# Performance work log

Hardware: AMD Instinct MI355X
Metric: run time of the kernel (lower is better)

## Reference

```python
import jax, jax.numpy as jnp
import numpy as np

MAX_ITER = 16
TOL = 1e-3


def setup_inputs() -> dict:
    key = jax.random.key(0)
    k0, k1, k2, k3 = jax.random.split(key, 4)
    B, A, Bd, Y = 16384, 1024, 2, 128
    AT = jax.random.uniform(k0, (B, A), dtype=jnp.float32)
    K = jax.random.uniform(k1, (A, Bd), dtype=jnp.float32)
    BT = jnp.ones((Bd,), dtype=jnp.float32)  # fixed to [1, 1] in the module
    u = jax.random.uniform(k2, (A * Bd, Y), dtype=jnp.float32)
    b = jax.random.uniform(k3, (Y,), dtype=jnp.float32)
    return {"AT": AT, "K": K, "BT": BT, "u": u, "b": b}


def reference(AT, K, BT, u, b):
    batch = AT.shape[0]
    Kp = K ** 2  # 'reparam' constraint

    # Fixed-point matrix-balancing loop (torch.no_grad block) -> constants.
    Ksg = jax.lax.stop_gradient(Kp)
    ATsg = jax.lax.stop_gradient(AT)
    A_dim, B_dim = Kp.shape
    af0 = jnp.zeros((batch, A_dim), jnp.float32)
    bf0 = jnp.zeros((batch, B_dim), jnp.float32)

    def cond(carry):
        _, _, err, i = carry
        return (i < MAX_ITER) & (err >= TOL)

    def body(carry):
        af, bf, _, i = carry
        af_n = ATsg / (bf @ Ksg.T + 1.0)   # (batch, A_dim)
        bf_n = BT / (af_n @ Ksg + 1.0)     # (batch, B_dim)
        err = jnp.max(jnp.abs(af_n - af)) + jnp.max(jnp.abs(bf_n - bf))
        return af_n, bf_n, err, i + 1

    _, bf, _, _ = jax.lax.while_loop(
        cond, body, (af0, bf0, jnp.array(jnp.inf, jnp.float32), 0)
    )
    bf = jax.lax.stop_gradient(bf)

    # Final differentiable iteration.
    af = AT / (bf @ Kp.T + 1.0)            # (batch, A_dim)
    bf = BT / (af @ Kp + 1.0)              # (batch, B_dim)

    # C = K * (AF @ BF^T): rank-1 outer product per batch element.
    C = (Kp[None, :, :] * af[:, :, None] * bf[:, None, :]).reshape(batch, -1)
    return C @ u + b
```

## Files before the change

### kernel.cpp

```cpp
#include <hip/hip_runtime.h>

__device__ __forceinline__ float b2f(unsigned short h) {
    unsigned int u = ((unsigned int)h) << 16;
    return __builtin_bit_cast(float, u);
}
__device__ __forceinline__ unsigned short f2b(float f) {
    unsigned int u = __builtin_bit_cast(unsigned int, f);
    u += 0x7fffu + ((u >> 16) & 1u);
    return (unsigned short)(u >> 16);
}

typedef short bf16x8_t __attribute__((ext_vector_type(8)));
typedef float f32x4_t  __attribute__((ext_vector_type(4)));

#define LDS_PTR(p) ((__attribute__((address_space(3))) void*)(p))
#define GLB_PTR(p) ((const __attribute__((address_space(1))) void*)(p))

#define NB   16384
#define AD   1024
#define YD   128
#define ND   256

__global__ __launch_bounds__(256) void vt_kernel(
    const float* __restrict__ Kq,
    const float* __restrict__ U,
    unsigned short* __restrict__ Vt)
{
    int idx = blockIdx.x * 256 + threadIdx.x;
    int n = idx >> 10;
    int a = idx & 1023;
    int j = n >> 7;
    int y = n & 127;
    float k  = Kq[2 * a + j];
    float kp = k * k;
    float uv = U[(size_t)(2 * a + j) * YD + y];
    Vt[idx] = f2b(kp * uv);
}

__global__ __launch_bounds__(256) void row_kernel(
    const float* __restrict__ AT,
    const float* __restrict__ Kq,
    const float* __restrict__ BTv,
    unsigned short* __restrict__ afb,
    float* __restrict__ bff)
{
    int wid  = blockIdx.x * 4 + (threadIdx.x >> 6);
    int lane = threadIdx.x & 63;
    const float* at = AT + (size_t)wid * AD;

    float ta[16], kp0[16], kp1[16];
#pragma unroll
    for (int c = 0; c < 4; ++c) {
        int base = c * 256 + lane * 4;
        float4 av = *(const float4*)(at + base);
        ta[c * 4 + 0] = av.x; ta[c * 4 + 1] = av.y;
        ta[c * 4 + 2] = av.z; ta[c * 4 + 3] = av.w;
        float4 k0 = *(const float4*)(Kq + 2 * base);
        float4 k1 = *(const float4*)(Kq + 2 * base + 4);
        kp0[c * 4 + 0] = k0.x * k0.x; kp1[c * 4 + 0] = k0.y * k0.y;
        kp0[c * 4 + 1] = k0.z * k0.z; kp1[c * 4 + 1] = k0.w * k0.w;
        kp0[c * 4 + 2] = k1.x * k1.x; kp1[c * 4 + 2] = k1.y * k1.y;
        kp0[c * 4 + 3] = k1.z * k1.z; kp1[c * 4 + 3] = k1.w * k1.w;
    }

    float M[9];
#pragma unroll
    for (int i = 0; i < 9; ++i) M[i] = 0.f;
#pragma unroll
    for (int e = 0; e < 16; ++e) {
        float t = ta[e], p = kp0[e], q = kp1[e];
        float u0 = t * p, u1 = t * q;
        M[0] += u0; M[1] += u1;
        float u00 = u0 * p, u01 = u0 * q, u11 = u1 * q;
        M[2] += u00; M[3] += u01; M[4] += u11;
        M[5] += u00 * p; M[6] += u00 * q; M[7] += u01 * q; M[8] += u11 * q;
    }
#pragma unroll
    for (int i = 0; i < 9; ++i) {
        for (int m = 1; m < 64; m <<= 1) M[i] += __shfl_xor(M[i], m, 64);
    }

    float bt0 = BTv[0], bt1 = BTv[1];
    float bf0 = 0.f, bf1 = 0.f;
#pragma unroll
    for (int it = 0; it < 8; ++it) {
        float q00 = bf0 * bf0, q01 = bf0 * bf1, q11 = bf1 * bf1;
        float s0 = M[0] - (bf0 * M[2] + bf1 * M[3]) + (q00 * M[5] + 2.f * q01 * M[6] + q11 * M[7]);
        float s1 = M[1] - (bf0 * M[3] + bf1 * M[4]) + (q00 * M[6] + 2.f * q01 * M[7] + q11 * M[8]);
        bf0 = bt0 / (1.f + s0);
        bf1 = bt1 / (1.f + s1);
    }
    if (lane == 0) { bff[(size_t)wid * 2] = bf0; bff[(size_t)wid * 2 + 1] = bf1; }

    unsigned short* ao = afb + (size_t)wid * AD;
#pragma unroll
    for (int c = 0; c < 4; ++c) {
        unsigned short r[4];
#pragma unroll
        for (int e = 0; e < 4; ++e) {
            int idx = c * 4 + e;
            r[e] = f2b(ta[idx] / (1.f + bf0 * kp0[idx] + bf1 * kp1[idx]));
        }
        *(ushort4*)(ao + c * 256 + lane * 4) = make_ushort4(r[0], r[1], r[2], r[3]);
    }
}

__global__ __launch_bounds__(256) void gemm_kernel(
    const unsigned short* __restrict__ Ag,
    const unsigned short* __restrict__ Bg,
    float* __restrict__ G)
{
    __shared__ __align__(16) unsigned short lA[128 * 64];
    __shared__ __align__(16) unsigned short lB[128 * 64];

    const int t = threadIdx.x;
    const int lane = t & 63;
    const int wave = t >> 6;
    const int wm = wave >> 1, wn = wave & 1;
    const int mtile = blockIdx.x, ntile = blockIdx.y;

    f32x4_t acc[4][4];
#pragma unroll
    for (int i = 0; i < 4; ++i)
#pragma unroll
        for (int j = 0; j < 4; ++j) acc[i][j] = (f32x4_t){0.f, 0.f, 0.f, 0.f};

    const unsigned short* gA[4];
    const unsigned short* gB[4];
    int ls[4];
#pragma unroll
    for (int i = 0; i < 4; ++i) {
        int s = i * 256 + t;
        int m = s >> 3;
        int c = (s & 7) ^ (m & 7);
        gA[i] = Ag + (size_t)(mtile * 128 + m) * AD + 8 * c;
        gB[i] = Bg + (size_t)(ntile * 128 + m) * AD + 8 * c;
        ls[i] = s * 8;
    }

    for (int k0 = 0; k0 < AD; k0 += 64) {
#pragma unroll
        for (int i = 0; i < 4; ++i) {
            __builtin_amdgcn_global_load_lds(GLB_PTR(gA[i] + k0), LDS_PTR(&lA[ls[i]]), 16, 0, 0);
            __builtin_amdgcn_global_load_lds(GLB_PTR(gB[i] + k0), LDS_PTR(&lB[ls[i]]), 16, 0, 0);
        }
        __syncthreads();
#pragma unroll
        for (int kk = 0; kk < 2; ++kk) {
            const int cq = kk * 4 + (lane >> 4);
            const int rr = lane & 15;
            bf16x8_t fa[4], fb[4];
#pragma unroll
            for (int i = 0; i < 4; ++i) {
                int m = wm * 64 + i * 16 + rr;
                fa[i] = *(const bf16x8_t*)(&lA[(m * 8 + (cq ^ (m & 7))) * 8]);
                int n = wn * 64 + i * 16 + rr;
                fb[i] = *(const bf16x8_t*)(&lB[(n * 8 + (cq ^ (n & 7))) * 8]);
            }
#pragma unroll
            for (int i = 0; i < 4; ++i)
#pragma unroll
                for (int j = 0; j < 4; ++j)
                    acc[i][j] = __builtin_amdgcn_mfma_f32_16x16x32_bf16(fa[i], fb[j], acc[i][j], 0, 0, 0);
        }
        __syncthreads();
    }

    const int q = lane >> 4, col = lane & 15;
#pragma unroll
    for (int i = 0; i < 4; ++i) {
        int mg = mtile * 128 + wm * 64 + i * 16 + q * 4;
#pragma unroll
        for (int j = 0; j < 4; ++j) {
            int ng = ntile * 128 + wn * 64 + j * 16 + col;
            float* gp = G + (size_t)mg * ND + ng;
#pragma unroll
            for (int r = 0; r < 4; ++r) gp[(size_t)r * ND] = acc[i][j][r];
        }
    }
}

__global__ __launch_bounds__(256) void combine_kernel(
    const float* __restrict__ G,
    const float* __restrict__ bff,
    const float* __restrict__ bias,
    float* __restrict__ out)
{
    int idx = blockIdx.x * 256 + threadIdx.x;
    int b  = idx >> 5;
    int y4 = (idx & 31) * 4;
    float bf0 = bff[2 * b], bf1 = bff[2 * b + 1];
    float4 g0 = *(const float4*)(G + (size_t)b * ND + y4);
    float4 g1 = *(const float4*)(G + (size_t)b * ND + YD + y4);
    float4 bv = *(const float4*)(bias + y4);
    float4 r;
    r.x = bf0 * g0.x + bf1 * g1.x + bv.x;
    r.y = bf0 * g0.y + bf1 * g1.y + bv.y;
    r.z = bf0 * g0.z + bf1 * g1.z + bv.z;
    r.w = bf0 * g0.w + bf1 * g1.w + bv.w;
    *(float4*)(out + (size_t)b * YD + y4) = r;
}

extern "C" void kernel_launch(void* const* d_in, const int* in_sizes, int n_in,
                              void* d_out, int out_size, void* d_ws, size_t ws_size,
                              hipStream_t stream) {
    const float* AT  = (const float*)d_in[0];
    const float* Kq  = (const float*)d_in[1];
    const float* BTv = (const float*)d_in[2];
    const float* U   = (const float*)d_in[3];
    const float* bia = (const float*)d_in[4];
    float* out = (float*)d_out;

    char* ws = (char*)d_ws;
    unsigned short* afb = (unsigned short*)(ws);
    unsigned short* Vt  = (unsigned short*)(ws + 33554432);
    float*          G   = (float*)(ws + 34078720);
    float*          bff = (float*)(ws + 50855936);

    vt_kernel<<<dim3(1024), dim3(256), 0, stream>>>(Kq, U, Vt);
    row_kernel<<<dim3(NB / 4), dim3(256), 0, stream>>>(AT, Kq, BTv, afb, bff);
    gemm_kernel<<<dim3(NB / 128, ND / 128), dim3(256), 0, stream>>>(afb, Vt, G);
    combine_kernel<<<dim3(NB * 32 / 256), dim3(256), 0, stream>>>(G, bff, bia, out);
}
```

Before: 140.6 us.

## Fuse combine epilogue into GEMM with full-N tiles per block

The GEMM now uses 32-row M tiles that span all 256 N columns, so each block holds both halves (j=0 and j=1) for the same output column. This lets it apply the bf weighting and bias in the epilogue and write the final output directly. The separate combine kernel and the 16 MB G intermediate round trip are removed. In exchange, every block reloads the full 256x1024 B matrix (likely served from L2), and each wave issues fewer MFMAs per LDS load, which lowers arithmetic intensity.

New measurement: 129.8 us. 7.7% less time.

```diff
diff --git a/kernel.cpp b/kernel.cpp
--- a/kernel.cpp
+++ b/kernel.cpp
@@ -105,60 +105,66 @@
     }
 }
 
-__global__ __launch_bounds__(256) void gemm_kernel(
+__global__ __launch_bounds__(256) void gemm_fused_kernel(
     const unsigned short* __restrict__ Ag,
     const unsigned short* __restrict__ Bg,
-    float* __restrict__ G)
+    const float* __restrict__ bff,
+    const float* __restrict__ bias,
+    float* __restrict__ out)
 {
-    __shared__ __align__(16) unsigned short lA[128 * 64];
-    __shared__ __align__(16) unsigned short lB[128 * 64];
+    __shared__ __align__(16) unsigned short lA[32 * 64];
+    __shared__ __align__(16) unsigned short lB[256 * 64];
 
     const int t = threadIdx.x;
     const int lane = t & 63;
-    const int wave = t >> 6;
-    const int wm = wave >> 1, wn = wave & 1;
-    const int mtile = blockIdx.x, ntile = blockIdx.y;
-
-    f32x4_t acc[4][4];
-#pragma unroll
-    for (int i = 0; i < 4; ++i)
+    const int wn = t >> 6;
+    const int mtile = blockIdx.x;
+
+    f32x4_t acc[2][4];
+#pragma unroll
+    for (int i = 0; i < 2; ++i)
 #pragma unroll
         for (int j = 0; j < 4; ++j) acc[i][j] = (f32x4_t){0.f, 0.f, 0.f, 0.f};
 
-    const unsigned short* gA[4];
-    const unsigned short* gB[4];
-    int ls[4];
-#pragma unroll
-    for (int i = 0; i < 4; ++i) {
-        int s = i * 256 + t;
+    const unsigned short* gA;
+    const unsigned short* gB[8];
+    {
+        int s = t;
         int m = s >> 3;
         int c = (s & 7) ^ (m & 7);
-        gA[i] = Ag + (size_t)(mtile * 128 + m) * AD + 8 * c;
-        gB[i] = Bg + (size_t)(ntile * 128 + m) * AD + 8 * c;
-        ls[i] = s * 8;
+        gA = Ag + (size_t)(mtile * 32 + m) * AD + 8 * c;
+    }
+#pragma unroll
+    for (int i = 0; i < 8; ++i) {
+        int s = i * 256 + t;
+        int n = s >> 3;
+        int c = (s & 7) ^ (n & 7);
+        gB[i] = Bg + (size_t)n * AD + 8 * c;
     }
 
     for (int k0 = 0; k0 < AD; k0 += 64) {
-#pragma unroll
-        for (int i = 0; i < 4; ++i) {
-            __builtin_amdgcn_global_load_lds(GLB_PTR(gA[i] + k0), LDS_PTR(&lA[ls[i]]), 16, 0, 0);
-            __builtin_amdgcn_global_load_lds(GLB_PTR(gB[i] + k0), LDS_PTR(&lB[ls[i]]), 16, 0, 0);
-        }
+        __builtin_amdgcn_global_load_lds(GLB_PTR(gA + k0), LDS_PTR(&lA[t * 8]), 16, 0, 0);
+#pragma unroll
+        for (int i = 0; i < 8; ++i)
+            __builtin_amdgcn_global_load_lds(GLB_PTR(gB[i] + k0), LDS_PTR(&lB[(i * 256 + t) * 8]), 16, 0, 0);
         __syncthreads();
 #pragma unroll
         for (int kk = 0; kk < 2; ++kk) {
             const int cq = kk * 4 + (lane >> 4);
             const int rr = lane & 15;
-            bf16x8_t fa[4], fb[4];
-#pragma unroll
-            for (int i = 0; i < 4; ++i) {
-                int m = wm * 64 + i * 16 + rr;
+            bf16x8_t fa[2], fb[4];
+#pragma unroll
+            for (int i = 0; i < 2; ++i) {
+                int m = i * 16 + rr;
                 fa[i] = *(const bf16x8_t*)(&lA[(m * 8 + (cq ^ (m & 7))) * 8]);
-                int n = wn * 64 + i * 16 + rr;
-                fb[i] = *(const bf16x8_t*)(&lB[(n * 8 + (cq ^ (n & 7))) * 8]);
             }
 #pragma unroll
-            for (int i = 0; i < 4; ++i)
+            for (int j = 0; j < 4; ++j) {
+                int n = wn * 32 + (j & 1) * 16 + (j >> 1) * 128 + rr;
+                fb[j] = *(const bf16x8_t*)(&lB[(n * 8 + (cq ^ (n & 7))) * 8]);
+            }
+#pragma unroll
+            for (int i = 0; i < 2; ++i)
 #pragma unroll
                 for (int j = 0; j < 4; ++j)
                     acc[i][j] = __builtin_amdgcn_mfma_f32_16x16x32_bf16(fa[i], fb[j], acc[i][j], 0, 0, 0);
@@ -168,37 +174,23 @@
 
     const int q = lane >> 4, col = lane & 15;
 #pragma unroll
-    for (int i = 0; i < 4; ++i) {
-        int mg = mtile * 128 + wm * 64 + i * 16 + q * 4;
-#pragma unroll
-        for (int j = 0; j < 4; ++j) {
-            int ng = ntile * 128 + wn * 64 + j * 16 + col;
-            float* gp = G + (size_t)mg * ND + ng;
-#pragma unroll
-            for (int r = 0; r < 4; ++r) gp[(size_t)r * ND] = acc[i][j][r];
+    for (int i = 0; i < 2; ++i) {
+        int mbase = mtile * 32 + i * 16 + q * 4;
+        float2 bfv[4];
+#pragma unroll
+        for (int r = 0; r < 4; ++r)
+            bfv[r] = *(const float2*)(bff + (size_t)(mbase + r) * 2);
+#pragma unroll
+        for (int j = 0; j < 2; ++j) {
+            int y = wn * 32 + j * 16 + col;
+            float bv = bias[y];
+#pragma unroll
+            for (int r = 0; r < 4; ++r) {
+                float val = bfv[r].x * acc[i][j][r] + bfv[r].y * acc[i][j + 2][r] + bv;
+                out[(size_t)(mbase + r) * YD + y] = val;
+            }
         }
     }
-}
-
-__global__ __launch_bounds__(256) void combine_kernel(
-    const float* __restrict__ G,
-    const float* __restrict__ bff,
-    const float* __restrict__ bias,
-    float* __restrict__ out)
-{
-    int idx = blockIdx.x * 256 + threadIdx.x;
-    int b  = idx >> 5;
-    int y4 = (idx & 31) * 4;
-    float bf0 = bff[2 * b], bf1 = bff[2 * b + 1];
-    float4 g0 = *(const float4*)(G + (size_t)b * ND + y4);
-    float4 g1 = *(const float4*)(G + (size_t)b * ND + YD + y4);
-    float4 bv = *(const float4*)(bias + y4);
-    float4 r;
-    r.x = bf0 * g0.x + bf1 * g1.x + bv.x;
-    r.y = bf0 * g0.y + bf1 * g1.y + bv.y;
-    r.z = bf0 * g0.z + bf1 * g1.z + bv.z;
-    r.w = bf0 * g0.w + bf1 * g1.w + bv.w;
-    *(float4*)(out + (size_t)b * YD + y4) = r;
 }
 
 extern "C" void kernel_launch(void* const* d_in, const int* in_sizes, int n_in,
@@ -214,11 +206,9 @@
     char* ws = (char*)d_ws;
     unsigned short* afb = (unsigned short*)(ws);
     unsigned short* Vt  = (unsigned short*)(ws + 33554432);
-    float*          G   = (float*)(ws + 34078720);
-    float*          bff = (float*)(ws + 50855936);
+    float*          bff = (float*)(ws + 34078720);
 
     vt_kernel<<<dim3(1024), dim3(256), 0, stream>>>(Kq, U, Vt);
     row_kernel<<<dim3(NB / 4), dim3(256), 0, stream>>>(AT, Kq, BTv, afb, bff);
-    gemm_kernel<<<dim3(NB / 128, ND / 128), dim3(256), 0, stream>>>(afb, Vt, G);
-    combine_kernel<<<dim3(NB * 32 / 256), dim3(256), 0, stream>>>(G, bff, bia, out);
-}
+    gemm_fused_kernel<<<dim3(NB / 32), dim3(256), 0, stream>>>(afb, Vt, bff, bia, out);
+}
```
